# Kernel tuning notes

Measured on AMD Instinct MI355X. Metric: run time of the kernel, lower is better.

Reference implementation:

```python
import jax, jax.numpy as jnp
import numpy as np

B, L, D, F = 1, 4096, 4096, 11008
# (start, end, side): side 0 = vision expert, side 1 = language expert.
# Mirrors merge_section_size over alternating contiguous vision/language token ranges.
SEGMENTS = [(0, 1024, 0), (1024, 2048, 1), (2048, 3072, 0), (3072, 4096, 1)]


def setup_inputs() -> dict:
    key = jax.random.key(0)
    ks = jax.random.split(key, 7)
    s = 0.02  # weight init scale
    hidden_states = jax.random.normal(ks[0], (B, L, D), jnp.float32)
    tt = np.zeros((B, L), np.int32)
    for a, b, side in SEGMENTS:
        tt[:, a:b] = side
    token_type_ids = jnp.asarray(tt)
    lg_w = jax.random.normal(ks[1], (D, F), jnp.float32) * s
    lu_w = jax.random.normal(ks[2], (D, F), jnp.float32) * s
    ld_w = jax.random.normal(ks[3], (F, D), jnp.float32) * s
    vg_w = jax.random.normal(ks[4], (D, F), jnp.float32) * s
    vu_w = jax.random.normal(ks[5], (D, F), jnp.float32) * s
    vd_w = jax.random.normal(ks[6], (F, D), jnp.float32) * s
    return {
        'hidden_states': hidden_states,
        'token_type_ids': token_type_ids,
        'lg_w': lg_w, 'lu_w': lu_w, 'ld_w': ld_w,
        'vg_w': vg_w, 'vu_w': vu_w, 'vd_w': vd_w,
    }


def _swiglu_mlp(x, gw, uw, dw):
    # x: [B, T, D] -> [B, T, D]; down(silu(gate(x)) * up(x))
    h = jax.nn.silu(jnp.einsum('btd,df->btf', x, gw)) * jnp.einsum('btd,df->btf', x, uw)
    return jnp.einsum('btf,fd->btd', h, dw)


def reference(hidden_states, token_type_ids, lg_w, lu_w, ld_w, vg_w, vu_w, vd_w):
    # Split-dispatch over static contiguous segments, then concat along seq dim.
    outs = []
    for a, b, side in SEGMENTS:
        seg = hidden_states[:, a:b, :]
        if side == 1:
            outs.append(_swiglu_mlp(seg, lg_w, lu_w, ld_w))
        else:
            outs.append(_swiglu_mlp(seg, vg_w, vu_w, vd_w))
    return jnp.concatenate(outs, axis=1)
```

## Files before the change

### kernel.cpp

```cpp
#include <hip/hip_runtime.h>
#include <math.h>

typedef unsigned short u16;
typedef short s16x8 __attribute__((ext_vector_type(8)));
typedef float f32x4 __attribute__((ext_vector_type(4)));

#define GLOAD16(gp, lp)                                                        \
  __builtin_amdgcn_global_load_lds(                                            \
      (const __attribute__((address_space(1))) void*)(gp),                     \
      (__attribute__((address_space(3))) void*)(lp), 16, 0, 0)

__device__ __forceinline__ u16 f2bf(float f) {
  union { float f; unsigned u; } v; v.f = f;
  unsigned r = v.u + 0x7fffu + ((v.u >> 16) & 1u);
  return (u16)(r >> 16);
}

__global__ __launch_bounds__(256) void cvt_x_kernel(const float* __restrict__ in,
                                                    u16* __restrict__ out) {
  size_t i = ((size_t)blockIdx.x * 256 + threadIdx.x) * 8;
  float4 a = *(const float4*)(in + i);
  float4 b = *(const float4*)(in + i + 4);
  s16x8 v;
  v[0] = (short)f2bf(a.x); v[1] = (short)f2bf(a.y);
  v[2] = (short)f2bf(a.z); v[3] = (short)f2bf(a.w);
  v[4] = (short)f2bf(b.x); v[5] = (short)f2bf(b.y);
  v[6] = (short)f2bf(b.z); v[7] = (short)f2bf(b.w);
  *(s16x8*)(out + i) = v;
}

__global__ __launch_bounds__(256) void transpose_cvt_kernel(
    const float* __restrict__ in0, const float* __restrict__ in1,
    const float* __restrict__ in2, const float* __restrict__ in3,
    const float* __restrict__ in4, const float* __restrict__ in5,
    u16* __restrict__ o0, u16* __restrict__ o1, u16* __restrict__ o2,
    u16* __restrict__ o3, u16* __restrict__ o4, u16* __restrict__ o5) {
  __shared__ float s[64 * 65];
  const int mat = blockIdx.y;
  const float* in; u16* out;
  switch (mat) {
    case 0: in = in0; out = o0; break;
    case 1: in = in1; out = o1; break;
    case 2: in = in2; out = o2; break;
    case 3: in = in3; out = o3; break;
    case 4: in = in4; out = o4; break;
    default: in = in5; out = o5; break;
  }
  const int R = (mat < 4) ? 4096 : 11008;
  const int C = (mat < 4) ? 11008 : 4096;
  const int nTc = C >> 6;
  const int tr = blockIdx.x / nTc, tc = blockIdx.x - tr * nTc;
  const int r0 = tr << 6, c0 = tc << 6;
  const int t = threadIdx.x;
#pragma unroll
  for (int p = 0; p < 4; ++p) {
    const int lr = p * 16 + (t >> 4);
    const int lc = (t & 15) * 4;
    float4 v = *(const float4*)(in + (size_t)(r0 + lr) * C + (c0 + lc));
    float* sp = &s[lr * 65 + lc];
    sp[0] = v.x; sp[1] = v.y; sp[2] = v.z; sp[3] = v.w;
  }
  __syncthreads();
#pragma unroll
  for (int q = 0; q < 2; ++q) {
    const int oc = q * 32 + (t >> 3);
    const int orr = (t & 7) * 8;
    s16x8 v;
#pragma unroll
    for (int i = 0; i < 8; ++i) v[i] = (short)f2bf(s[(orr + i) * 65 + oc]);
    *(s16x8*)(out + (size_t)(c0 + oc) * R + (r0 + orr)) = v;
  }
}

__global__ __launch_bounds__(256, 2) void gemm_gateup_kernel(
    const u16* __restrict__ X, const u16* __restrict__ GTl,
    const u16* __restrict__ UTl, const u16* __restrict__ GTv,
    const u16* __restrict__ UTv, const int* __restrict__ tt,
    u16* __restrict__ H) {
  __shared__ u16 sA[128 * 64];
  __shared__ u16 sG[128 * 64];
  __shared__ u16 sU[128 * 64];

  const int mT = blockIdx.x & 31;
  const int nT = blockIdx.x >> 5;
  const int t = threadIdx.x;
  const int lane = t & 63;
  const int wr = ((t >> 7) & 1) * 64;
  const int wc = ((t >> 6) & 1) * 64;

  const int side = tt[mT << 7];
  const u16* GT = side ? GTl : GTv;
  const u16* UT = side ? UTl : UTv;

  const int swz = (((t & 7) ^ ((t >> 3) & 7)) << 4);
  const char* aP = (const char*)X  + (size_t)((mT << 7) + (t >> 3)) * 8192 + swz;
  const char* gP = (const char*)GT + (size_t)((nT << 7) + (t >> 3)) * 8192 + swz;
  const char* uP = (const char*)UT + (size_t)((nT << 7) + (t >> 3)) * 8192 + swz;
  const int ldsOff = (t & 192) << 4;

  f32x4 accG[4][4], accU[4][4];
  const f32x4 z = {0.f, 0.f, 0.f, 0.f};
#pragma unroll
  for (int i = 0; i < 4; ++i)
#pragma unroll
    for (int j = 0; j < 4; ++j) { accG[i][j] = z; accU[i][j] = z; }

  const int hi16 = ((lane >> 4) << 4);
  const int rsw = (lane & 7) << 4;
  const int rlo = lane & 15;

  for (int kk = 0; kk < 64; ++kk) {
#pragma unroll
    for (int p = 0; p < 4; ++p) {
      GLOAD16(aP + (size_t)p * 262144, (char*)sA + (p << 12) + ldsOff);
      GLOAD16(gP + (size_t)p * 262144, (char*)sG + (p << 12) + ldsOff);
      GLOAD16(uP + (size_t)p * 262144, (char*)sU + (p << 12) + ldsOff);
    }
    aP += 128; gP += 128; uP += 128;
    __syncthreads();
#pragma unroll
    for (int ks = 0; ks < 2; ++ks) {
      s16x8 af[4], gf[4], uf[4];
      const int kb = (ks << 6) + hi16;
#pragma unroll
      for (int i = 0; i < 4; ++i) {
        const int ra = (wr + i * 16 + rlo) * 128 + (kb ^ rsw);
        af[i] = *(const s16x8*)((const char*)sA + ra);
        const int rb = (wc + i * 16 + rlo) * 128 + (kb ^ rsw);
        gf[i] = *(const s16x8*)((const char*)sG + rb);
        uf[i] = *(const s16x8*)((const char*)sU + rb);
      }
#pragma unroll
      for (int i = 0; i < 4; ++i)
#pragma unroll
        for (int j = 0; j < 4; ++j) {
          accG[i][j] = __builtin_amdgcn_mfma_f32_16x16x32_bf16(af[i], gf[j], accG[i][j], 0, 0, 0);
          accU[i][j] = __builtin_amdgcn_mfma_f32_16x16x32_bf16(af[i], uf[j], accU[i][j], 0, 0, 0);
        }
    }
    __syncthreads();
  }

  const int r0 = (mT << 7) + wr + ((lane >> 4) << 2);
  const int c0 = (nT << 7) + wc + rlo;
#pragma unroll
  for (int i = 0; i < 4; ++i)
#pragma unroll
    for (int j = 0; j < 4; ++j)
#pragma unroll
      for (int r = 0; r < 4; ++r) {
        const float g = accG[i][j][r];
        const float u = accU[i][j][r];
        const float hv = g / (1.f + __expf(-g)) * u;
        H[(size_t)(r0 + i * 16 + r) * 11008 + (c0 + j * 16)] = f2bf(hv);
      }
}

__global__ __launch_bounds__(256, 2) void gemm_down_kernel(
    const u16* __restrict__ H, const u16* __restrict__ DTl,
    const u16* __restrict__ DTv, const int* __restrict__ tt,
    float* __restrict__ out) {
  __shared__ u16 sA[128 * 64];
  __shared__ u16 sB[128 * 64];

  const int mT = blockIdx.x & 31;
  const int nT = blockIdx.x >> 5;
  const int t = threadIdx.x;
  const int lane = t & 63;
  const int wr = ((t >> 7) & 1) * 64;
  const int wc = ((t >> 6) & 1) * 64;

  const int side = tt[mT << 7];
  const u16* DT = side ? DTl : DTv;

  const int swz = (((t & 7) ^ ((t >> 3) & 7)) << 4);
  const char* aP = (const char*)H  + (size_t)((mT << 7) + (t >> 3)) * 22016 + swz;
  const char* bP = (const char*)DT + (size_t)((nT << 7) + (t >> 3)) * 22016 + swz;
  const int ldsOff = (t & 192) << 4;

  f32x4 acc[4][4];
  const f32x4 z = {0.f, 0.f, 0.f, 0.f};
#pragma unroll
  for (int i = 0; i < 4; ++i)
#pragma unroll
    for (int j = 0; j < 4; ++j) acc[i][j] = z;

  const int hi16 = ((lane >> 4) << 4);
  const int rsw = (lane & 7) << 4;
  const int rlo = lane & 15;

  for (int kk = 0; kk < 172; ++kk) {
#pragma unroll
    for (int p = 0; p < 4; ++p) {
      GLOAD16(aP + (size_t)p * 704512, (char*)sA + (p << 12) + ldsOff);
      GLOAD16(bP + (size_t)p * 704512, (char*)sB + (p << 12) + ldsOff);
    }
    aP += 128; bP += 128;
    __syncthreads();
#pragma unroll
    for (int ks = 0; ks < 2; ++ks) {
      s16x8 af[4], bfr[4];
      const int kb = (ks << 6) + hi16;
#pragma unroll
      for (int i = 0; i < 4; ++i) {
        af[i] = *(const s16x8*)((const char*)sA + (wr + i * 16 + rlo) * 128 + (kb ^ rsw));
        bfr[i] = *(const s16x8*)((const char*)sB + (wc + i * 16 + rlo) * 128 + (kb ^ rsw));
      }
#pragma unroll
      for (int i = 0; i < 4; ++i)
#pragma unroll
        for (int j = 0; j < 4; ++j)
          acc[i][j] = __builtin_amdgcn_mfma_f32_16x16x32_bf16(af[i], bfr[j], acc[i][j], 0, 0, 0);
    }
    __syncthreads();
  }

  const int r0 = (mT << 7) + wr + ((lane >> 4) << 2);
  const int c0 = (nT << 7) + wc + rlo;
#pragma unroll
  for (int i = 0; i < 4; ++i)
#pragma unroll
    for (int j = 0; j < 4; ++j)
#pragma unroll
      for (int r = 0; r < 4; ++r)
        out[(size_t)(r0 + i * 16 + r) * 4096 + (c0 + j * 16)] = acc[i][j][r];
}

extern "C" void kernel_launch(void* const* d_in, const int* in_sizes, int n_in,
                              void* d_out, int out_size, void* d_ws, size_t ws_size,
                              hipStream_t stream) {
  (void)in_sizes; (void)n_in; (void)out_size; (void)ws_size;
  const float* x  = (const float*)d_in[0];
  const int*   tt = (const int*)d_in[1];
  const float* lg = (const float*)d_in[2];
  const float* lu = (const float*)d_in[3];
  const float* ld = (const float*)d_in[4];
  const float* vg = (const float*)d_in[5];
  const float* vu = (const float*)d_in[6];
  const float* vd = (const float*)d_in[7];

  u16* ws  = (u16*)d_ws;
  u16* xbf = ws;
  u16* lgT = xbf + 16777216;
  u16* luT = lgT + 45088768;
  u16* vgT = luT + 45088768;
  u16* vuT = vgT + 45088768;
  u16* ldT = vuT + 45088768;
  u16* vdT = ldT + 45088768;
  u16* hbuf = vdT + 45088768;

  cvt_x_kernel<<<dim3(8192), dim3(256), 0, stream>>>(x, xbf);
  transpose_cvt_kernel<<<dim3(11008, 6), dim3(256), 0, stream>>>(
      lg, lu, vg, vu, ld, vd, lgT, luT, vgT, vuT, ldT, vdT);
  gemm_gateup_kernel<<<dim3(2752), dim3(256), 0, stream>>>(
      xbf, lgT, luT, vgT, vuT, tt, hbuf);
  gemm_down_kernel<<<dim3(1024), dim3(256), 0, stream>>>(
      hbuf, ldT, vdT, tt, (float*)d_out);
}
```

Measured before the change: 1.508 ms.

## Replace GEMMs with 256x256 double-buffered pipelined kernel and interleaved gate/up weights

Gate and up weights are interleaved into one transposed matrix in 16-row groups, so the gate/up projection becomes a single GEMM whose adjacent output fragments hold paired gate/up values for the SiLU epilogue. Both GEMMs now use a shared templated 256x256-tile kernel with 512 threads and double-buffered LDS staging via global_load_lds. Its schedule interleaves loads with MFMA quadrants using explicit vmcnt waits, barriers and setprio, plus a workgroup index remap for cache locality. This targets global and LDS traffic per FLOP and hides load latency, at the cost of one block per CU and fewer blocks for the down GEMM (256).

```diff
diff --git a/kernel.cpp b/kernel.cpp
--- a/kernel.cpp
+++ b/kernel.cpp
@@ -33,16 +33,16 @@
     const float* __restrict__ in0, const float* __restrict__ in1,
     const float* __restrict__ in2, const float* __restrict__ in3,
     const float* __restrict__ in4, const float* __restrict__ in5,
-    u16* __restrict__ o0, u16* __restrict__ o1, u16* __restrict__ o2,
-    u16* __restrict__ o3, u16* __restrict__ o4, u16* __restrict__ o5) {
+    u16* __restrict__ o01, u16* __restrict__ o23,
+    u16* __restrict__ o4, u16* __restrict__ o5) {
   __shared__ float s[64 * 65];
   const int mat = blockIdx.y;
   const float* in; u16* out;
   switch (mat) {
-    case 0: in = in0; out = o0; break;
-    case 1: in = in1; out = o1; break;
-    case 2: in = in2; out = o2; break;
-    case 3: in = in3; out = o3; break;
+    case 0: in = in0; out = o01; break;
+    case 1: in = in1; out = o01; break;
+    case 2: in = in2; out = o23; break;
+    case 3: in = in3; out = o23; break;
     case 4: in = in4; out = o4; break;
     default: in = in5; out = o5; break;
   }
@@ -68,162 +68,211 @@
     s16x8 v;
 #pragma unroll
     for (int i = 0; i < 8; ++i) v[i] = (short)f2bf(s[(orr + i) * 65 + oc]);
-    *(s16x8*)(out + (size_t)(c0 + oc) * R + (r0 + orr)) = v;
-  }
-}
-
-__global__ __launch_bounds__(256, 2) void gemm_gateup_kernel(
-    const u16* __restrict__ X, const u16* __restrict__ GTl,
-    const u16* __restrict__ UTl, const u16* __restrict__ GTv,
-    const u16* __restrict__ UTv, const int* __restrict__ tt,
-    u16* __restrict__ H) {
-  __shared__ u16 sA[128 * 64];
-  __shared__ u16 sG[128 * 64];
-  __shared__ u16 sU[128 * 64];
-
-  const int mT = blockIdx.x & 31;
-  const int nT = blockIdx.x >> 5;
+    const int f = c0 + oc;
+    size_t orow;
+    if (mat < 4) orow = (size_t)((f >> 4) << 5) + ((mat & 1) << 4) + (f & 15);
+    else         orow = (size_t)f;
+    *(s16x8*)(out + orow * R + (r0 + orr)) = v;
+  }
+}
+
+template <int KB, int EPI>
+__global__ __launch_bounds__(512, 1) void gemm256(
+    const u16* __restrict__ A, const u16* __restrict__ Bl,
+    const u16* __restrict__ Bv, const int* __restrict__ tt,
+    void* __restrict__ OutP) {
+  constexpr int NK = KB / 128;
+  constexpr int L = NK / 2;
+  __shared__ u16 sA[2][2][128][64];
+  __shared__ u16 sB[2][2][128][64];
+
+  const int nwg = gridDim.x;
+  const int bid = blockIdx.x;
+  const int wg = (bid & 7) * (nwg >> 3) + (bid >> 3);
+  const int mT = wg & 15;
+  const int nT = wg >> 4;
+
   const int t = threadIdx.x;
   const int lane = t & 63;
-  const int wr = ((t >> 7) & 1) * 64;
-  const int wc = ((t >> 6) & 1) * 64;
-
-  const int side = tt[mT << 7];
-  const u16* GT = side ? GTl : GTv;
-  const u16* UT = side ? UTl : UTv;
-
-  const int swz = (((t & 7) ^ ((t >> 3) & 7)) << 4);
-  const char* aP = (const char*)X  + (size_t)((mT << 7) + (t >> 3)) * 8192 + swz;
-  const char* gP = (const char*)GT + (size_t)((nT << 7) + (t >> 3)) * 8192 + swz;
-  const char* uP = (const char*)UT + (size_t)((nT << 7) + (t >> 3)) * 8192 + swz;
-  const int ldsOff = (t & 192) << 4;
-
-  f32x4 accG[4][4], accU[4][4];
+  const int rlo = lane & 15;
+  const int hi = lane >> 4;
+  const int wn = (t >> 6) & 3;
+  const int wm = (t >> 8) & 1;
+
+  const int side = tt[mT << 8];
+  const u16* B = side ? Bl : Bv;
+
+  const int rowq = t >> 3;
+  const int gsw = ((t & 7) ^ (rowq & 7)) << 4;
+  const char* srcA = (const char*)A + (size_t)(mT * 256 + rowq) * KB + gsw;
+  const char* srcB = (const char*)B + (size_t)(nT * 256 + rowq) * KB + gsw;
+  char* ldsA = (char*)&sA[0][0][0][0];
+  char* ldsB = (char*)&sB[0][0][0][0];
+  const int woff = (t & 448) << 4;
+
+#define STG_A(d, h, kt)                                                        \
+  do {                                                                         \
+    GLOAD16(srcA + (size_t)((h) * 128) * KB + (kt) * 128,                      \
+            ldsA + (d) * 32768 + (h) * 16384 + woff);                          \
+    GLOAD16(srcA + (size_t)((h) * 128 + 64) * KB + (kt) * 128,                 \
+            ldsA + (d) * 32768 + (h) * 16384 + 8192 + woff);                   \
+  } while (0)
+#define STG_B(d, h, kt)                                                        \
+  do {                                                                         \
+    GLOAD16(srcB + (size_t)((h) * 128) * KB + (kt) * 128,                      \
+            ldsB + (d) * 32768 + (h) * 16384 + woff);                          \
+    GLOAD16(srcB + (size_t)((h) * 128 + 64) * KB + (kt) * 128,                 \
+            ldsB + (d) * 32768 + (h) * 16384 + 8192 + woff);                   \
+  } while (0)
+
+  const int cxa = (hi ^ (rlo & 7)) << 4;
+  const int cxb = ((4 + hi) ^ (rlo & 7)) << 4;
+  const int arow = (wm * 64 + rlo) * 128;
+  const int brow = (wn * 32 + rlo) * 128;
+
+  s16x8 af[4][2], bf[2][2];
+  f32x4 acc[8][4];
   const f32x4 z = {0.f, 0.f, 0.f, 0.f};
 #pragma unroll
-  for (int i = 0; i < 4; ++i)
-#pragma unroll
-    for (int j = 0; j < 4; ++j) { accG[i][j] = z; accU[i][j] = z; }
-
-  const int hi16 = ((lane >> 4) << 4);
-  const int rsw = (lane & 7) << 4;
-  const int rlo = lane & 15;
-
-  for (int kk = 0; kk < 64; ++kk) {
-#pragma unroll
-    for (int p = 0; p < 4; ++p) {
-      GLOAD16(aP + (size_t)p * 262144, (char*)sA + (p << 12) + ldsOff);
-      GLOAD16(gP + (size_t)p * 262144, (char*)sG + (p << 12) + ldsOff);
-      GLOAD16(uP + (size_t)p * 262144, (char*)sU + (p << 12) + ldsOff);
-    }
-    aP += 128; gP += 128; uP += 128;
-    __syncthreads();
-#pragma unroll
-    for (int ks = 0; ks < 2; ++ks) {
-      s16x8 af[4], gf[4], uf[4];
-      const int kb = (ks << 6) + hi16;
-#pragma unroll
-      for (int i = 0; i < 4; ++i) {
-        const int ra = (wr + i * 16 + rlo) * 128 + (kb ^ rsw);
-        af[i] = *(const s16x8*)((const char*)sA + ra);
-        const int rb = (wc + i * 16 + rlo) * 128 + (kb ^ rsw);
-        gf[i] = *(const s16x8*)((const char*)sG + rb);
-        uf[i] = *(const s16x8*)((const char*)sU + rb);
+  for (int i = 0; i < 8; ++i)
+#pragma unroll
+    for (int j = 0; j < 4; ++j) acc[i][j] = z;
+
+#define LDA(d, mh)                                                             \
+  do {                                                                         \
+    _Pragma("unroll") for (int fi = 0; fi < 4; ++fi) {                         \
+      const char* p = ldsA + (d) * 32768 + (mh) * 16384 + arow + fi * 2048;    \
+      af[fi][0] = *(const s16x8*)(p + cxa);                                    \
+      af[fi][1] = *(const s16x8*)(p + cxb);                                    \
+    }                                                                          \
+  } while (0)
+#define LDB(d, nh)                                                             \
+  do {                                                                         \
+    _Pragma("unroll") for (int gi = 0; gi < 2; ++gi) {                         \
+      const char* p = ldsB + (d) * 32768 + (nh) * 16384 + brow + gi * 2048;    \
+      bf[gi][0] = *(const s16x8*)(p + cxa);                                    \
+      bf[gi][1] = *(const s16x8*)(p + cxb);                                    \
+    }                                                                          \
+  } while (0)
+#define MFMA16(mh, nh)                                                         \
+  do {                                                                         \
+    __builtin_amdgcn_s_setprio(1);                                             \
+    _Pragma("unroll") for (int fi = 0; fi < 4; ++fi)                           \
+        _Pragma("unroll") for (int gi = 0; gi < 2; ++gi) {                     \
+      acc[(mh)*4 + fi][(nh)*2 + gi] = __builtin_amdgcn_mfma_f32_16x16x32_bf16( \
+          af[fi][0], bf[gi][0], acc[(mh)*4 + fi][(nh)*2 + gi], 0, 0, 0);       \
+      acc[(mh)*4 + fi][(nh)*2 + gi] = __builtin_amdgcn_mfma_f32_16x16x32_bf16( \
+          af[fi][1], bf[gi][1], acc[(mh)*4 + fi][(nh)*2 + gi], 0, 0, 0);       \
+    }                                                                          \
+    __builtin_amdgcn_s_setprio(0);                                             \
+  } while (0)
+#define SBAR() __builtin_amdgcn_s_barrier()
+#define VMCNT4() do { asm volatile("s_waitcnt vmcnt(4)" ::: "memory");         \
+                      __builtin_amdgcn_sched_barrier(0); } while (0)
+#define VMCNT0() do { asm volatile("s_waitcnt vmcnt(0)" ::: "memory");         \
+                      __builtin_amdgcn_sched_barrier(0); } while (0)
+
+  STG_A(0, 0, 0); STG_A(0, 1, 0); STG_B(0, 0, 0); STG_B(0, 1, 0);
+  STG_B(1, 0, 1); STG_A(1, 1, 1);
+  VMCNT4();
+  SBAR();
+
+  for (int it = 0; it < L - 1; ++it) {
+    const int T = 2 * it;
+    LDA(0, 0); LDB(0, 0);
+    STG_A(1, 0, T + 1); STG_B(1, 1, T + 1);
+    SBAR(); MFMA16(0, 0); SBAR();
+    LDA(0, 1);
+    SBAR(); MFMA16(1, 0); SBAR();
+    LDB(0, 1);
+    STG_B(0, 0, T + 2);
+    SBAR(); MFMA16(1, 1); SBAR();
+    LDA(0, 0);
+    STG_A(0, 1, T + 2);
+    SBAR(); MFMA16(0, 1);
+    VMCNT4(); SBAR();
+    LDA(1, 0); LDB(1, 0);
+    STG_A(0, 0, T + 2); STG_B(0, 1, T + 2);
+    SBAR(); MFMA16(0, 0); SBAR();
+    LDA(1, 1);
+    SBAR(); MFMA16(1, 0); SBAR();
+    LDB(1, 1);
+    STG_B(1, 0, T + 3);
+    SBAR(); MFMA16(1, 1); SBAR();
+    LDA(1, 0);
+    STG_A(1, 1, T + 3);
+    SBAR(); MFMA16(0, 1);
+    VMCNT4(); SBAR();
+  }
+  {
+    const int T = NK - 2;
+    LDA(0, 0); LDB(0, 0);
+    STG_A(1, 0, T + 1); STG_B(1, 1, T + 1);
+    SBAR(); MFMA16(0, 0); SBAR();
+    LDA(0, 1);
+    SBAR(); MFMA16(1, 0); SBAR();
+    LDB(0, 1);
+    SBAR(); MFMA16(1, 1); SBAR();
+    LDA(0, 0);
+    SBAR(); MFMA16(0, 1);
+    VMCNT0(); SBAR();
+    LDA(1, 0); LDB(1, 0);
+    SBAR(); MFMA16(0, 0); SBAR();
+    LDA(1, 1);
+    SBAR(); MFMA16(1, 0); SBAR();
+    LDB(1, 1);
+    SBAR(); MFMA16(1, 1); SBAR();
+    LDA(1, 0);
+    SBAR(); MFMA16(0, 1);
+  }
+
+  if (EPI == 0) {
+    u16* H = (u16*)OutP;
+#pragma unroll
+    for (int mh = 0; mh < 2; ++mh)
+#pragma unroll
+      for (int fi = 0; fi < 4; ++fi) {
+        const int row0 = mT * 256 + mh * 128 + wm * 64 + fi * 16 + hi * 4;
+#pragma unroll
+        for (int nh = 0; nh < 2; ++nh) {
+          const int fc = nT * 128 + (nh * 4 + wn) * 16 + rlo;
+          const f32x4 g = acc[mh * 4 + fi][nh * 2 + 0];
+          const f32x4 u = acc[mh * 4 + fi][nh * 2 + 1];
+#pragma unroll
+          for (int r = 0; r < 4; ++r) {
+            const float gv = g[r];
+            const float hv = gv / (1.f + __expf(-gv)) * u[r];
+            H[(size_t)(row0 + r) * 11008 + fc] = f2bf(hv);
+          }
+        }
       }
-#pragma unroll
-      for (int i = 0; i < 4; ++i)
-#pragma unroll
-        for (int j = 0; j < 4; ++j) {
-          accG[i][j] = __builtin_amdgcn_mfma_f32_16x16x32_bf16(af[i], gf[j], accG[i][j], 0, 0, 0);
-          accU[i][j] = __builtin_amdgcn_mfma_f32_16x16x32_bf16(af[i], uf[j], accU[i][j], 0, 0, 0);
-        }
-    }
-    __syncthreads();
-  }
-
-  const int r0 = (mT << 7) + wr + ((lane >> 4) << 2);
-  const int c0 = (nT << 7) + wc + rlo;
-#pragma unroll
-  for (int i = 0; i < 4; ++i)
-#pragma unroll
-    for (int j = 0; j < 4; ++j)
-#pragma unroll
-      for (int r = 0; r < 4; ++r) {
-        const float g = accG[i][j][r];
-        const float u = accU[i][j][r];
-        const float hv = g / (1.f + __expf(-g)) * u;
-        H[(size_t)(r0 + i * 16 + r) * 11008 + (c0 + j * 16)] = f2bf(hv);
+  } else {
+    float* O = (float*)OutP;
+#pragma unroll
+    for (int mh = 0; mh < 2; ++mh)
+#pragma unroll
+      for (int fi = 0; fi < 4; ++fi) {
+        const int row0 = mT * 256 + mh * 128 + wm * 64 + fi * 16 + hi * 4;
+#pragma unroll
+        for (int nh = 0; nh < 2; ++nh)
+#pragma unroll
+          for (int gi = 0; gi < 2; ++gi) {
+            const int col = nT * 256 + nh * 128 + wn * 32 + gi * 16 + rlo;
+            const f32x4 a = acc[mh * 4 + fi][nh * 2 + gi];
+#pragma unroll
+            for (int r = 0; r < 4; ++r)
+              O[(size_t)(row0 + r) * 4096 + col] = a[r];
+          }
       }
-}
-
-__global__ __launch_bounds__(256, 2) void gemm_down_kernel(
-    const u16* __restrict__ H, const u16* __restrict__ DTl,
-    const u16* __restrict__ DTv, const int* __restrict__ tt,
-    float* __restrict__ out) {
-  __shared__ u16 sA[128 * 64];
-  __shared__ u16 sB[128 * 64];
-
-  const int mT = blockIdx.x & 31;
-  const int nT = blockIdx.x >> 5;
-  const int t = threadIdx.x;
-  const int lane = t & 63;
-  const int wr = ((t >> 7) & 1) * 64;
-  const int wc = ((t >> 6) & 1) * 64;
-
-  const int side = tt[mT << 7];
-  const u16* DT = side ? DTl : DTv;
-
-  const int swz = (((t & 7) ^ ((t >> 3) & 7)) << 4);
-  const char* aP = (const char*)H  + (size_t)((mT << 7) + (t >> 3)) * 22016 + swz;
-  const char* bP = (const char*)DT + (size_t)((nT << 7) + (t >> 3)) * 22016 + swz;
-  const int ldsOff = (t & 192) << 4;
-
-  f32x4 acc[4][4];
-  const f32x4 z = {0.f, 0.f, 0.f, 0.f};
-#pragma unroll
-  for (int i = 0; i < 4; ++i)
-#pragma unroll
-    for (int j = 0; j < 4; ++j) acc[i][j] = z;
-
-  const int hi16 = ((lane >> 4) << 4);
-  const int rsw = (lane & 7) << 4;
-  const int rlo = lane & 15;
-
-  for (int kk = 0; kk < 172; ++kk) {
-#pragma unroll
-    for (int p = 0; p < 4; ++p) {
-      GLOAD16(aP + (size_t)p * 704512, (char*)sA + (p << 12) + ldsOff);
-      GLOAD16(bP + (size_t)p * 704512, (char*)sB + (p << 12) + ldsOff);
-    }
-    aP += 128; bP += 128;
-    __syncthreads();
-#pragma unroll
-    for (int ks = 0; ks < 2; ++ks) {
-      s16x8 af[4], bfr[4];
-      const int kb = (ks << 6) + hi16;
-#pragma unroll
-      for (int i = 0; i < 4; ++i) {
-        af[i] = *(const s16x8*)((const char*)sA + (wr + i * 16 + rlo) * 128 + (kb ^ rsw));
-        bfr[i] = *(const s16x8*)((const char*)sB + (wc + i * 16 + rlo) * 128 + (kb ^ rsw));
-      }
-#pragma unroll
-      for (int i = 0; i < 4; ++i)
-#pragma unroll
-        for (int j = 0; j < 4; ++j)
-          acc[i][j] = __builtin_amdgcn_mfma_f32_16x16x32_bf16(af[i], bfr[j], acc[i][j], 0, 0, 0);
-    }
-    __syncthreads();
-  }
-
-  const int r0 = (mT << 7) + wr + ((lane >> 4) << 2);
-  const int c0 = (nT << 7) + wc + rlo;
-#pragma unroll
-  for (int i = 0; i < 4; ++i)
-#pragma unroll
-    for (int j = 0; j < 4; ++j)
-#pragma unroll
-      for (int r = 0; r < 4; ++r)
-        out[(size_t)(r0 + i * 16 + r) * 4096 + (c0 + j * 16)] = acc[i][j][r];
+  }
+#undef STG_A
+#undef STG_B
+#undef LDA
+#undef LDB
+#undef MFMA16
+#undef SBAR
+#undef VMCNT4
+#undef VMCNT0
 }
 
 extern "C" void kernel_launch(void* const* d_in, const int* in_sizes, int n_in,
@@ -241,19 +290,15 @@
 
   u16* ws  = (u16*)d_ws;
   u16* xbf = ws;
-  u16* lgT = xbf + 16777216;
-  u16* luT = lgT + 45088768;
-  u16* vgT = luT + 45088768;
-  u16* vuT = vgT + 45088768;
-  u16* ldT = vuT + 45088768;
+  u16* GUl = xbf + 16777216;
+  u16* GUv = GUl + 90177536;
+  u16* ldT = GUv + 90177536;
   u16* vdT = ldT + 45088768;
   u16* hbuf = vdT + 45088768;
 
   cvt_x_kernel<<<dim3(8192), dim3(256), 0, stream>>>(x, xbf);
   transpose_cvt_kernel<<<dim3(11008, 6), dim3(256), 0, stream>>>(
-      lg, lu, vg, vu, ld, vd, lgT, luT, vgT, vuT, ldT, vdT);
-  gemm_gateup_kernel<<<dim3(2752), dim3(256), 0, stream>>>(
-      xbf, lgT, luT, vgT, vuT, tt, hbuf);
-  gemm_down_kernel<<<dim3(1024), dim3(256), 0, stream>>>(
-      hbuf, ldT, vdT, tt, (float*)d_out);
-}
+      lg, lu, vg, vu, ld, vd, GUl, GUv, ldT, vdT);
+  gemm256<8192, 0><<<dim3(1376), dim3(512), 0, stream>>>(xbf, GUl, GUv, tt, hbuf);
+  gemm256<22016, 1><<<dim3(256), dim3(512), 0, stream>>>(hbuf, ldT, vdT, tt, d_out);
+}
```

Result: no change. 1.520 ms (+0.8%).
